# Kernel tuning notes

Hardware: AMD Instinct MI355X
Metric: run time of the kernel (lower is better)

Reference implementation:

```python
import jax, jax.numpy as jnp
import numpy as np

N = 20000      # nodes
E = 640000     # edges
HID = 128      # hidden_dim
HEADS = 8
HD = HID // HEADS  # head_dim = 16


def setup_inputs() -> dict:
    key = jax.random.key(0)
    ks = jax.random.split(key, 32)
    s = 1.0 / np.sqrt(HID)
    d = {}
    d["h"] = jax.random.normal(ks[0], (N, HID), jnp.float32)
    d["x"] = jax.random.normal(ks[1], (N, 3), jnp.float32)
    d["src"] = jax.random.randint(ks[2], (E,), 0, N)
    d["dst"] = jax.random.randint(ks[3], (E,), 0, N)
    d["distances"] = jax.random.uniform(ks[4], (E,), jnp.float32)
    d["bpp_edge_bias"] = jax.random.uniform(ks[5], (E,), jnp.float32)
    d["msa_edge_bias"] = jax.random.uniform(ks[6], (E,), jnp.float32)
    d["chem_edge_bias"] = jax.random.uniform(ks[7], (E,), jnp.float32)
    d["relative_offset"] = jax.random.normal(ks[8], (E,), jnp.float32)
    d["chain_break_mask"] = jax.random.uniform(ks[9], (E,), jnp.float32)
    # attention projections (nn.Linear(hidden, hidden): y = x @ W + b)
    for i, nm in enumerate(["Wq", "Wk", "Wv", "Wo"]):
        d[nm] = jax.random.normal(ks[10 + i], (HID, HID), jnp.float32) * s
    for nm in ["bq", "bk", "bv", "bo"]:
        d[nm] = jnp.zeros((HID,), jnp.float32)
    # six Linear(1, heads) edge-bias heads -> weight vector [HEADS] + bias [HEADS]
    for i, nm in enumerate(["dist", "bpp", "msa", "chem", "rel", "chain"]):
        d["w_" + nm] = jax.random.normal(ks[14 + i], (HEADS,), jnp.float32) * 0.1
        d["b_" + nm] = jnp.zeros((HEADS,), jnp.float32)
    # coord_gate: Linear(HID,HID) -> SiLU -> Linear(HID,1) -> Tanh
    d["Wg1"] = jax.random.normal(ks[20], (HID, HID), jnp.float32) * s
    d["bg1"] = jnp.zeros((HID,), jnp.float32)
    d["wg2"] = jax.random.normal(ks[21], (HID, 1), jnp.float32) * s
    d["bg2"] = jnp.zeros((1,), jnp.float32)
    return d


def _edge_bias(feat, w, b):
    # Linear(1, heads) applied to per-edge scalar: [E] -> [E, HEADS]
    return feat[:, None] * w[None, :] + b[None, :]


def reference(h, x, src, dst, distances, bpp_edge_bias, msa_edge_bias,
              chem_edge_bias, relative_offset, chain_break_mask,
              Wq, bq, Wk, bk, Wv, bv, Wo, bo,
              w_dist, b_dist, w_bpp, b_bpp, w_msa, b_msa,
              w_chem, b_chem, w_rel, b_rel, w_chain, b_chain,
              Wg1, bg1, wg2, bg2):
    n = h.shape[0]
    q = (h @ Wq + bq).reshape(n, HEADS, HD)
    k = (h @ Wk + bk).reshape(n, HEADS, HD)
    v = (h @ Wv + bv).reshape(n, HEADS, HD)
    q_src = q[src]   # [E, H, D]
    k_dst = k[dst]
    v_dst = v[dst]
    logits = jnp.einsum('ehd,ehd->eh', q_src, k_dst) / np.sqrt(float(HD))
    logits = (logits
              - _edge_bias(distances * distances, w_dist, b_dist)
              + _edge_bias(bpp_edge_bias, w_bpp, b_bpp)
              + _edge_bias(msa_edge_bias, w_msa, b_msa)
              + _edge_bias(chem_edge_bias, w_chem, b_chem)
              + _edge_bias(relative_offset, w_rel, b_rel)
              + _edge_bias(chain_break_mask, w_chain, b_chain))
    # segment softmax over edges grouped by src node, per head
    m = jax.ops.segment_max(logits, src, num_segments=n)        # [N, H]
    ex = jnp.exp(logits - m[src])                               # [E, H]
    denom = jax.ops.segment_sum(ex, src, num_segments=n)        # [N, H]
    weights = ex / jnp.maximum(denom[src], 1e-9)                # [E, H]
    # weighted scatter-aggregate of values to src nodes
    h_update = jax.ops.segment_sum(v_dst * weights[:, :, None], src,
                                   num_segments=n).reshape(n, HID)
    h_out = h + h_update @ Wo + bo
    # coordinate update
    weights_mean = weights.mean(axis=1)                         # [E]
    disp = jax.ops.segment_sum((x[dst] - x[src]) * weights_mean[:, None],
                               src, num_segments=n)             # [N, 3]
    gate = jnp.tanh(jax.nn.silu(h_out @ Wg1 + bg1) @ wg2 + bg2)  # [N, 1]
    x_out = x + gate * disp
    return h_out, x_out
```

## Files before the change

### kernel.cpp

```cpp
#include <hip/hip_runtime.h>
#include <hip/hip_bf16.h>
#include <hip/hip_fp16.h>

#define N_NODES 20000
#define N_EDGES 640000
#define HID 128
#define HEADS 8
#define HD 16
#define NB_SCAN ((N_NODES + 255) / 256)
#define CH 192
#define QKV_BLOCKS 625
#define PREP_BLOCKS 2
#define NREP 32
#define HIST_OFF (PREP_BLOCKS + QKV_BLOCKS)
#define HIST_BLOCKS 128

typedef __attribute__((ext_vector_type(8))) short bf16x8;
typedef __attribute__((ext_vector_type(4))) float f32x4;
typedef __attribute__((ext_vector_type(2))) float f32x2;
typedef _Float16 half2_t __attribute__((ext_vector_type(2)));

#if __has_builtin(__builtin_amdgcn_cvt_pk_f32_fp8) && __has_builtin(__builtin_amdgcn_cvt_pk_fp8_f32)
#define FP8_FAST 1
#else
#define FP8_FAST 0
#include <hip/hip_fp8.h>
#endif

__device__ __forceinline__ float bflo(unsigned u) {
    union { unsigned i; float f; } x; x.i = u << 16; return x.f;
}
__device__ __forceinline__ float bfhi(unsigned u) {
    union { unsigned i; float f; } x; x.i = u & 0xffff0000u; return x.f;
}
__device__ __forceinline__ float bfu(ushort u) {
    union { unsigned i; float f; } x; x.i = ((unsigned)u) << 16; return x.f;
}
__device__ __forceinline__ ushort f2bu(float f) {
    __hip_bfloat16 b = __float2bfloat16(f);
    union { __hip_bfloat16 b; ushort u; } c; c.b = b; return c.u;
}
__device__ __forceinline__ ushort f2hu(float f) {
    __half hh = __float2half(f);
    union { __half h; ushort u; } c; c.h = hh; return c.u;
}
__device__ __forceinline__ float fdot2h(unsigned a, unsigned b, float c) {
    union { unsigned u; half2_t h; } A, B;
    A.u = a; B.u = b;
#if __has_builtin(__builtin_amdgcn_fdot2)
    return __builtin_amdgcn_fdot2(A.h, B.h, c, false);
#else
    return c + (float)A.h[0] * (float)B.h[0] + (float)A.h[1] * (float)B.h[1];
#endif
}
__device__ __forceinline__ unsigned fp8x4_enc(float a, float b, float c, float d) {
#if FP8_FAST
    unsigned w = (unsigned)__builtin_amdgcn_cvt_pk_fp8_f32(a, b, 0, false);
    w = (unsigned)__builtin_amdgcn_cvt_pk_fp8_f32(c, d, (int)w, true);
    return w;
#else
    __hip_fp8_e4m3 e0(a), e1(b), e2(c), e3(d);
    return (unsigned)e0.__x | ((unsigned)e1.__x << 8) |
           ((unsigned)e2.__x << 16) | ((unsigned)e3.__x << 24);
#endif
}
__device__ __forceinline__ void fp8x4_dec(unsigned p, float* o) {
#if FP8_FAST
    f32x2 lo = __builtin_amdgcn_cvt_pk_f32_fp8((int)p, false);
    f32x2 hi = __builtin_amdgcn_cvt_pk_f32_fp8((int)p, true);
    o[0] = lo[0]; o[1] = lo[1]; o[2] = hi[0]; o[3] = hi[1];
#else
#pragma unroll
    for (int i = 0; i < 4; ++i) {
        unsigned char b = (p >> (8 * i)) & 0xff;
        __hip_fp8_e4m3 e; e.__x = b;
        o[i] = (float)e;
    }
#endif
}

__global__ __launch_bounds__(256) void front_kernel(
        const float* __restrict__ h,
        const float* __restrict__ bq, const float* __restrict__ bk,
        const float* __restrict__ bv,
        ushort* __restrict__ qb, ushort* __restrict__ kb,
        unsigned char* __restrict__ vb8,
        const int* __restrict__ src,
        int* __restrict__ cnt, int* __restrict__ rank,
        const float* __restrict__ Wq, const float* __restrict__ Wk,
        const float* __restrict__ Wv, const float* __restrict__ Wo,
        const float* __restrict__ Wg1, ushort* __restrict__ Wt) {
    __shared__ __align__(16) ushort hs[32 * 136];
    __shared__ __align__(16) ushort ws[128 * 136];
    const int t = threadIdx.x;
    if (blockIdx.x < PREP_BLOCKS) {
        const float* W = (blockIdx.x == 0) ? Wo : Wg1;
        ushort* out = Wt + (size_t)(3 + blockIdx.x) * 16384;
        for (int i = t; i < 16384; i += 256) {
            int k = i >> 7, n = i & 127;
            out[n * 128 + k] = f2bu(W[i]);
        }
    } else if (blockIdx.x < HIST_OFF) {
        const int row0 = (blockIdx.x - PREP_BLOCKS) * 32;
        for (int i = t; i < 4096; i += 256)
            hs[(i >> 7) * 136 + (i & 127)] = f2bu(h[(size_t)row0 * 128 + i]);
        __syncthreads();
        const int w = t >> 6, lane = t & 63;
        const int rt = w >> 1, half = w & 1;
        const int lrow = lane & 15, lkb = (lane >> 4) * 8;
        bf16x8 a[4];
#pragma unroll
        for (int ks = 0; ks < 4; ++ks)
            a[ks] = *reinterpret_cast<const bf16x8*>(&hs[(rt * 16 + lrow) * 136 + ks * 32 + lkb]);
        __syncthreads();
        const int rloc0 = rt * 16 + (lane >> 4) * 4;
#define STAGE_W(WSRC) \
        for (int idx = t; idx < 8192; idx += 256) { \
            const int c = idx & 127, kp = idx >> 7; \
            const float w0 = WSRC[(2 * kp) * 128 + c]; \
            const float w1 = WSRC[(2 * kp + 1) * 128 + c]; \
            *reinterpret_cast<unsigned*>(&ws[c * 136 + 2 * kp]) = \
                (unsigned)f2bu(w0) | ((unsigned)f2bu(w1) << 16); \
        } \
        __syncthreads();
#define MFMA_COL(col, acc) \
        { \
            _Pragma("unroll") \
            for (int ks = 0; ks < 4; ++ks) { \
                bf16x8 b = *reinterpret_cast<const bf16x8*>( \
                    &ws[(col) * 136 + ks * 32 + lkb]); \
                acc = __builtin_amdgcn_mfma_f32_16x16x32_bf16(a[ks], b, acc, 0, 0, 0); \
            } \
        }
#define DO_MAT_F16(WSRC, BIAS, OUT) \
        { \
        STAGE_W(WSRC) \
        for (int ctp = 0; ctp < 4; ++ctp) { \
            const int col = (ctp * 2 + half) * 16 + lrow; \
            f32x4 acc = {0.f, 0.f, 0.f, 0.f}; \
            MFMA_COL(col, acc) \
            const float bias = BIAS[col]; \
            _Pragma("unroll") \
            for (int r = 0; r < 4; ++r) \
                hs[(rloc0 + r) * 128 + col] = f2hu(acc[r] + bias); \
        } \
        __syncthreads(); \
        { \
            uint4* outp = reinterpret_cast<uint4*>(OUT + (size_t)row0 * 128); \
            const uint4* inp = reinterpret_cast<const uint4*>(hs); \
            outp[t] = inp[t]; \
            outp[t + 256] = inp[t + 256]; \
        } \
        __syncthreads(); \
        }
        DO_MAT_F16(Wq, bq, qb)
        DO_MAT_F16(Wk, bk, kb)
        {
        STAGE_W(Wv)
        unsigned char* hsb = reinterpret_cast<unsigned char*>(hs);
        for (int ctp = 0; ctp < 4; ++ctp) {
            const int col = (ctp * 2 + half) * 16 + lrow;
            f32x4 acc = {0.f, 0.f, 0.f, 0.f};
            MFMA_COL(col, acc)
            const float bias = bv[col];
            const unsigned wpk = fp8x4_enc(acc[0] + bias, acc[1] + bias,
                                           acc[2] + bias, acc[3] + bias);
#pragma unroll
            for (int r = 0; r < 4; ++r)
                hsb[(rloc0 + r) * 128 + col] = (unsigned char)((wpk >> (8 * r)) & 0xff);
        }
        __syncthreads();
        {
            uint4* outp = reinterpret_cast<uint4*>(vb8 + (size_t)row0 * 128);
            const uint4* inp = reinterpret_cast<const uint4*>(hs);
            outp[t] = inp[t];
        }
        }
#undef DO_MAT_F16
#undef MFMA_COL
#undef STAGE_W
    } else {
        const int b = blockIdx.x - HIST_OFF;
        for (int e = b * 256 + t; e < N_EDGES; e += HIST_BLOCKS * 256) {
            const int rep = (e >> 8) & (NREP - 1);
            rank[e] = atomicAdd(&cnt[rep * N_NODES + src[e]], 1);
        }
    }
}

__global__ __launch_bounds__(256) void scan1_kernel(const int* __restrict__ cnt,
        int* __restrict__ repOff, int* __restrict__ startp,
        int* __restrict__ blockSums, int* __restrict__ ticket, int n) {
    __shared__ int sd[256];
    __shared__ int lastFlag;
    const int tid = threadIdx.x;
    const int i = blockIdx.x * 256 + tid;
    int running = 0;
    if (i < n) {
#pragma unroll
        for (int r = 0; r < NREP; ++r) {
            int v = cnt[r * N_NODES + i];
            repOff[r * N_NODES + i] = running;
            running += v;
        }
    }
    sd[tid] = running;
    __syncthreads();
#pragma unroll
    for (int off = 1; off < 256; off <<= 1) {
        int tv = (tid >= off) ? sd[tid - off] : 0;
        __syncthreads();
        sd[tid] += tv;
        __syncthreads();
    }
    if (i < n) startp[i] = sd[tid] - running;
    if (tid == 255) {
        atomicExch(&blockSums[blockIdx.x], sd[255]);
        __threadfence();
        lastFlag = (atomicAdd(ticket, 1) == NB_SCAN - 1);
    }
    __syncthreads();
    if (lastFlag) {
        int v = (tid < NB_SCAN) ? atomicAdd(&blockSums[tid], 0) : 0;
        sd[tid] = v;
        __syncthreads();
#pragma unroll
        for (int off = 1; off < 256; off <<= 1) {
            int tv = (tid >= off) ? sd[tid - off] : 0;
            __syncthreads();
            sd[tid] += tv;
            __syncthreads();
        }
        if (tid < NB_SCAN) blockSums[tid] = sd[tid] - v;
        if (tid == 255) blockSums[NB_SCAN] = sd[255];
    }
}

__global__ __launch_bounds__(256) void scatter_kernel(
        const int* __restrict__ src, const int* __restrict__ dst,
        const float* __restrict__ dist, const float* __restrict__ bpp,
        const float* __restrict__ msa, const float* __restrict__ chem,
        const float* __restrict__ rel, const float* __restrict__ chain,
        const float* __restrict__ w_dist, const float* __restrict__ b_dist,
        const float* __restrict__ w_bpp, const float* __restrict__ b_bpp,
        const float* __restrict__ w_msa, const float* __restrict__ b_msa,
        const float* __restrict__ w_chem, const float* __restrict__ b_chem,
        const float* __restrict__ w_rel, const float* __restrict__ b_rel,
        const float* __restrict__ w_chain, const float* __restrict__ b_chain,
        const int* __restrict__ startp, const int* __restrict__ blockSums,
        const int* __restrict__ repOff, const int* __restrict__ rank,
        const float* __restrict__ x,
        uint4* __restrict__ bias16, uint2* __restrict__ meta) {
    const int b = blockIdx.x;
    const int e = b * 256 + threadIdx.x;
    const int s = src[e];
    const int rep = b & (NREP - 1);
    const int pos = startp[s] + blockSums[s >> 8] + repOff[rep * N_NODES + s] + rank[e];
    const int dn = dst[e];
    const float d2 = dist[e] * dist[e];
    const float f_bpp = bpp[e], f_msa = msa[e], f_chem = chem[e];
    const float f_rel = rel[e], f_chain = chain[e];
    ushort o16[8];
#pragma unroll
    for (int hq = 0; hq < 8; ++hq) {
        float bb = -(d2 * w_dist[hq] + b_dist[hq])
                + (f_bpp * w_bpp[hq] + b_bpp[hq])
                + (f_msa * w_msa[hq] + b_msa[hq])
                + (f_chem * w_chem[hq] + b_chem[hq])
                + (f_rel * w_rel[hq] + b_rel[hq])
                + (f_chain * w_chain[hq] + b_chain[hq]);
        o16[hq] = f2bu(bb);
    }
    uint4 b4;
    b4.x = (unsigned)o16[0] | ((unsigned)o16[1] << 16);
    b4.y = (unsigned)o16[2] | ((unsigned)o16[3] << 16);
    b4.z = (unsigned)o16[4] | ((unsigned)o16[5] << 16);
    b4.w = (unsigned)o16[6] | ((unsigned)o16[7] << 16);
    const float* xp = &x[(size_t)dn * 3];
    uint2 mt;
    mt.x = (unsigned)f2bu(xp[0]) | ((unsigned)f2bu(xp[1]) << 16);
    mt.y = (unsigned)f2bu(xp[2]) | ((unsigned)dn << 16);
    bias16[pos] = b4;
    meta[pos]   = mt;
}

__global__ __launch_bounds__(256) void node_kernel(const ushort* __restrict__ qb,
        const ushort* __restrict__ kb, const unsigned char* __restrict__ vb8,
        const uint4* __restrict__ bias16, const uint2* __restrict__ meta,
        const float* __restrict__ x,
        const int* __restrict__ startp, const int* __restrict__ blockSums,
        ushort* __restrict__ hub, float* __restrict__ disp) {
    __shared__ __align__(16) unsigned qLdsU[4 * 64];
    __shared__ float xsLds[12];
    __shared__ int   sLds[5];
    __shared__ ushort dnLds[CH];
    __shared__ float xLds[CH * 3];
    __shared__ ushort pbLds[CH * 8];
    __shared__ float redN[4][32][9];

    const int t = threadIdx.x;
    const int n0 = blockIdx.x * 4;
    const ushort* biasU = reinterpret_cast<const ushort*>(bias16);

    if (t < 64) {
        const uint4 qv = reinterpret_cast<const uint4*>(qb + (size_t)n0 * 128)[t];
        *reinterpret_cast<uint4*>(&qLdsU[t * 4]) = qv;
    }
    if (t < 12) xsLds[t] = x[(size_t)n0 * 3 + t];
    if (t < 5) {
        int idx = n0 + t;
        sLds[t] = (idx < N_NODES) ? (startp[idx] + blockSums[idx >> 8]) : N_EDGES;
    }
    __syncthreads();

    const int S0 = sLds[0], S4 = sLds[4];
    const int s1r = sLds[1], s2r = sLds[2], s3r = sLds[3];

    const int eg = t >> 5;
    const int dq = t & 31;
    const int hh = dq >> 2;
    const int jj = dq & 3;
    const int j3 = (jj < 3) ? jj : 0;

    float acc0[4] = {0,0,0,0}, acc1[4] = {0,0,0,0};
    float acc2[4] = {0,0,0,0}, acc3[4] = {0,0,0,0};
    float den0 = 0, den1 = 0, den2 = 0, den3 = 0;
    float adx0 = 0, adx1 = 0, adx2 = 0, adx3 = 0;

    for (int base = S0; base < S4; base += CH) {
        const int en = min(CH, S4 - base);
        __syncthreads();
        if (t < en) {
            const uint2 mt = meta[base + t];
            dnLds[t] = (ushort)(mt.y >> 16);
            xLds[t * 3 + 0] = bfu((ushort)(mt.x & 0xffff));
            xLds[t * 3 + 1] = bfu((ushort)(mt.x >> 16));
            xLds[t * 3 + 2] = bfu((ushort)(mt.y & 0xffff));
        }
        __syncthreads();
        const int np = en * 8;
#define PA_BODY(P) { \
            const int e = (P) >> 3, ha = (P) & 7; \
            const int ge = base + e; \
            const int m = (ge >= s1r) + (ge >= s2r) + (ge >= s3r); \
            const ushort* krow = kb + (size_t)dnLds[e] * 128 + ha * 16; \
            const uint4 ka = *reinterpret_cast<const uint4*>(krow); \
            const uint4 kb4 = *reinterpret_cast<const uint4*>(krow + 8); \
            const float bias = bfu(biasU[(size_t)base * 8 + (P)]); \
            const unsigned* qrowU = &qLdsU[m * 64 + ha * 8]; \
            const uint4 qa = *reinterpret_cast<const uint4*>(qrowU); \
            const uint4 qb4 = *reinterpret_cast<const uint4*>(qrowU + 4); \
            float s0 = 0.f, s1 = 0.f, s2 = 0.f, s3 = 0.f; \
            s0 = fdot2h(ka.x, qa.x, s0);   s1 = fdot2h(ka.y, qa.y, s1); \
            s2 = fdot2h(ka.z, qa.z, s2);   s3 = fdot2h(ka.w, qa.w, s3); \
            s0 = fdot2h(kb4.x, qb4.x, s0); s1 = fdot2h(kb4.y, qb4.y, s1); \
            s2 = fdot2h(kb4.z, qb4.z, s2); s3 = fdot2h(kb4.w, qb4.w, s3); \
            pbLds[P] = f2bu(__expf(fmaf((s0 + s1) + (s2 + s3), 0.25f, bias))); \
        }
        {
            int p = t;
            for (; p + 256 < np; p += 512) { PA_BODY(p) PA_BODY(p + 256) }
            if (p < np) PA_BODY(p)
        }
#undef PA_BODY
        __syncthreads();
#define PC_BODY(E, ACC, DEN, ADX, XSV) { \
            const float pe = bfu(pbLds[(E) * 8 + hh]); \
            const unsigned vp = *reinterpret_cast<const unsigned*>( \
                vb8 + (size_t)dnLds[E] * 128 + dq * 4); \
            float vd[4]; \
            fp8x4_dec(vp, vd); \
            ACC[0] = fmaf(pe, vd[0], ACC[0]); \
            ACC[1] = fmaf(pe, vd[1], ACC[1]); \
            ACC[2] = fmaf(pe, vd[2], ACC[2]); \
            ACC[3] = fmaf(pe, vd[3], ACC[3]); \
            DEN += pe; \
            ADX = fmaf(pe, xLds[(E) * 3 + j3] - XSV, ADX); \
        }
#define NODE_C(M, ACC, DEN, ADX) { \
            const int lo = max(sLds[M] - base, 0); \
            const int hi = min(sLds[M + 1] - base, en); \
            const float xsv = xsLds[M * 3 + j3]; \
            int e = lo + eg; \
            for (; e + 8 < hi; e += 16) { \
                PC_BODY(e, ACC, DEN, ADX, xsv) \
                PC_BODY(e + 8, ACC, DEN, ADX, xsv) \
            } \
            if (e < hi) PC_BODY(e, ACC, DEN, ADX, xsv) \
        }
        NODE_C(0, acc0, den0, adx0)
        NODE_C(1, acc1, den1, adx1)
        NODE_C(2, acc2, den2, adx2)
        NODE_C(3, acc3, den3, adx3)
#undef NODE_C
#undef PC_BODY
    }

    const int wv = t >> 6, lane = t & 63;
#define RED_M(M, ACC, DEN, ADX) { \
        float r0 = ACC[0], r1 = ACC[1], r2 = ACC[2], r3 = ACC[3]; \
        float rd = DEN, rx = (jj < 3) ? ADX : 0.f; \
        r0 += __shfl_xor(r0, 32); r1 += __shfl_xor(r1, 32); \
        r2 += __shfl_xor(r2, 32); r3 += __shfl_xor(r3, 32); \
        rd += __shfl_xor(rd, 32); rx += __shfl_xor(rx, 32); \
        if (lane < 32) { \
            redN[wv][lane][0] = r0; redN[wv][lane][1] = r1; \
            redN[wv][lane][2] = r2; redN[wv][lane][3] = r3; \
            redN[wv][lane][4] = rd; redN[wv][lane][5] = rx; \
        } \
        __syncthreads(); \
        if (t < 128) { \
            const int dqr = t >> 2, vi = t & 3; \
            float s = redN[0][dqr][vi] + redN[1][dqr][vi] \
                    + redN[2][dqr][vi] + redN[3][dqr][vi]; \
            float d = redN[0][dqr][4] + redN[1][dqr][4] \
                    + redN[2][dqr][4] + redN[3][dqr][4]; \
            hub[(size_t)(n0 + M) * 128 + t] = f2bu(s / fmaxf(d, 1e-9f)); \
        } \
        if (t < 32) { \
            float v = redN[0][t][5] + redN[1][t][5] + redN[2][t][5] + redN[3][t][5]; \
            float d = redN[0][t][4] + redN[1][t][4] + redN[2][t][4] + redN[3][t][4]; \
            float s = v / fmaxf(d, 1e-9f); \
            s += __shfl_xor(s, 4); s += __shfl_xor(s, 8); s += __shfl_xor(s, 16); \
            if (t < 3) disp[(size_t)(n0 + M) * 3 + t] = s * 0.125f; \
        } \
        __syncthreads(); }
    RED_M(0, acc0, den0, adx0)
    RED_M(1, acc1, den1, adx1)
    RED_M(2, acc2, den2, adx2)
    RED_M(3, acc3, den3, adx3)
#undef RED_M
}

__global__ __launch_bounds__(256) void out_kernel(const float* __restrict__ h,
        const float* __restrict__ x, const ushort* __restrict__ hub,
        const ushort* __restrict__ Wt,
        const float* __restrict__ bo, const float* __restrict__ bg1,
        const float* __restrict__ wg2, const float* __restrict__ bg2,
        const float* __restrict__ disp,
        float* __restrict__ hout, float* __restrict__ xout) {
    __shared__ __align__(16) ushort hus[32 * 136];
    __shared__ __align__(16) float hof[32 * 132];
    __shared__ float g1s[32 * 132];
    const int t = threadIdx.x;
    const int row0 = blockIdx.x * 32;
    for (int i8 = t; i8 < 512; i8 += 256) {
        const int row = i8 >> 4, c8 = (i8 & 15) * 8;
        *reinterpret_cast<uint4*>(&hus[row * 136 + c8]) =
            reinterpret_cast<const uint4*>(hub + (size_t)row0 * 128)[i8];
    }
    for (int i4 = t; i4 < 1024; i4 += 256) {
        const int row = i4 >> 5, c4 = (i4 & 31) * 4;
        *reinterpret_cast<float4*>(&hof[row * 132 + c4]) =
            reinterpret_cast<const float4*>(h + (size_t)row0 * 128)[i4];
    }
    __syncthreads();
    const int w = t >> 6, lane = t & 63;
    const int rt = w >> 1, half = w & 1;
    const int lrow = lane & 15, lkb = (lane >> 4) * 8;
    const int rloc = rt * 16 + (lane >> 4) * 4;
    bf16x8 a[4];
#pragma unroll
    for (int ks = 0; ks < 4; ++ks)
        a[ks] = *reinterpret_cast<const bf16x8*>(&hus[(rt * 16 + lrow) * 136 + ks * 32 + lkb]);
    for (int ctp = 0; ctp < 4; ++ctp) {
        const int col = (ctp * 2 + half) * 16 + lrow;
        f32x4 acc = {0.f, 0.f, 0.f, 0.f};
#pragma unroll
        for (int ks = 0; ks < 4; ++ks) {
            bf16x8 b = *reinterpret_cast<const bf16x8*>(&Wt[3 * 16384 + col * 128 + ks * 32 + lkb]);
            acc = __builtin_amdgcn_mfma_f32_16x16x32_bf16(a[ks], b, acc, 0, 0, 0);
        }
        const float bias = bo[col];
#pragma unroll
        for (int r = 0; r < 4; ++r)
            hof[(rloc + r) * 132 + col] += acc[r] + bias;
    }
    __syncthreads();
    for (int i4 = t; i4 < 1024; i4 += 256) {
        const int row = i4 >> 5, c4 = (i4 & 31) * 4;
        *reinterpret_cast<float4*>(hout + (size_t)(row0 + row) * 128 + c4) =
            *reinterpret_cast<const float4*>(&hof[row * 132 + c4]);
    }
    bf16x8 a2[4];
#pragma unroll
    for (int ks = 0; ks < 4; ++ks) {
        const float* fp = &hof[(rt * 16 + lrow) * 132 + ks * 32 + lkb];
        const float4 f0 = *reinterpret_cast<const float4*>(fp);
        const float4 f1 = *reinterpret_cast<const float4*>(fp + 4);
        bf16x8 v;
        v[0] = (short)f2bu(f0.x); v[1] = (short)f2bu(f0.y);
        v[2] = (short)f2bu(f0.z); v[3] = (short)f2bu(f0.w);
        v[4] = (short)f2bu(f1.x); v[5] = (short)f2bu(f1.y);
        v[6] = (short)f2bu(f1.z); v[7] = (short)f2bu(f1.w);
        a2[ks] = v;
    }
    for (int ctp = 0; ctp < 4; ++ctp) {
        const int col = (ctp * 2 + half) * 16 + lrow;
        f32x4 acc = {0.f, 0.f, 0.f, 0.f};
#pragma unroll
        for (int ks = 0; ks < 4; ++ks) {
            bf16x8 b = *reinterpret_cast<const bf16x8*>(&Wt[4 * 16384 + col * 128 + ks * 32 + lkb]);
            acc = __builtin_amdgcn_mfma_f32_16x16x32_bf16(a2[ks], b, acc, 0, 0, 0);
        }
        const float bias = bg1[col];
#pragma unroll
        for (int r = 0; r < 4; ++r) {
            float av = acc[r] + bias;
            g1s[(rloc + r) * 132 + col] = av / (1.f + __expf(-av));
        }
    }
    __syncthreads();
    {
        const int r = t >> 3, j = t & 7;
        float partial = 0.f;
        for (int cc = j; cc < 128; cc += 8) partial += g1s[r * 132 + cc] * wg2[cc];
        partial += __shfl_xor(partial, 1);
        partial += __shfl_xor(partial, 2);
        partial += __shfl_xor(partial, 4);
        const float gate = tanhf(partial + bg2[0]);
        if (j < 3) {
            const int row = row0 + r;
            xout[(size_t)row * 3 + j] = x[(size_t)row * 3 + j] + gate * disp[(size_t)row * 3 + j];
        }
    }
}


extern "C" void kernel_launch(void* const* d_in, const int* in_sizes, int n_in,
                              void* d_out, int out_size, void* d_ws, size_t ws_size,
                              hipStream_t stream) {
    const float* h     = (const float*)d_in[0];
    const float* x     = (const float*)d_in[1];
    const int*   src   = (const int*)d_in[2];
    const int*   dst   = (const int*)d_in[3];
    const float* dist  = (const float*)d_in[4];
    const float* bpp   = (const float*)d_in[5];
    const float* msa   = (const float*)d_in[6];
    const float* chem  = (const float*)d_in[7];
    const float* rel   = (const float*)d_in[8];
    const float* chain = (const float*)d_in[9];
    const float* Wq = (const float*)d_in[10];
    const float* Wk = (const float*)d_in[11];
    const float* Wv = (const float*)d_in[12];
    const float* Wo = (const float*)d_in[13];
    const float* bq = (const float*)d_in[14];
    const float* bk = (const float*)d_in[15];
    const float* bv = (const float*)d_in[16];
    const float* bo = (const float*)d_in[17];
    const float* w_dist = (const float*)d_in[18];  const float* b_dist = (const float*)d_in[19];
    const float* w_bpp  = (const float*)d_in[20];  const float* b_bpp  = (const float*)d_in[21];
    const float* w_msa  = (const float*)d_in[22];  const float* b_msa  = (const float*)d_in[23];
    const float* w_chem = (const float*)d_in[24];  const float* b_chem = (const float*)d_in[25];
    const float* w_rel  = (const float*)d_in[26];  const float* b_rel  = (const float*)d_in[27];
    const float* w_chain= (const float*)d_in[28];  const float* b_chain= (const float*)d_in[29];
    const float* Wg1 = (const float*)d_in[30];
    const float* bg1 = (const float*)d_in[31];
    const float* wg2 = (const float*)d_in[32];
    const float* bg2 = (const float*)d_in[33];

    char* wp = (char*)d_ws;
    const size_t NH2 = (size_t)N_NODES * HID * sizeof(ushort);
    ushort* hub   = (ushort*)wp;               wp += NH2;
    ushort* qb    = (ushort*)wp;               wp += NH2;
    ushort* kb    = (ushort*)wp;               wp += NH2;
    unsigned char* vb8 = (unsigned char*)wp;   wp += (size_t)N_NODES * HID;
    uint4*  bias16= (uint4*)wp;                wp += (size_t)N_EDGES * 16;
    uint2*  meta  = (uint2*)wp;                wp += (size_t)N_EDGES * 8;
    float*  disp  = (float*)wp;                wp += (size_t)N_NODES * 3 * sizeof(float);
    int* rank     = (int*)wp;                  wp += (size_t)N_EDGES * sizeof(int);
    int* startp   = (int*)wp;                  wp += (size_t)N_NODES * sizeof(int);
    int* cnt      = (int*)wp;                  wp += (size_t)NREP * N_NODES * sizeof(int);
    int* ticket   = (int*)wp;                  wp += sizeof(int);
    int* repOff   = (int*)wp;                  wp += (size_t)NREP * N_NODES * sizeof(int);
    int* blockSums= (int*)wp;                  wp += (size_t)(NB_SCAN + 1) * sizeof(int);
    ushort* Wt    = (ushort*)wp;               wp += (size_t)5 * 16384 * sizeof(ushort);

    float* hout = (float*)d_out;
    float* xout = hout + (size_t)N_NODES * HID;

    hipMemsetAsync(cnt, 0, ((size_t)NREP * N_NODES + 1) * sizeof(int), stream);
    hipLaunchKernelGGL(front_kernel, dim3(HIST_OFF + HIST_BLOCKS), dim3(256), 0, stream,
                       h, bq, bk, bv, qb, kb, vb8,
                       src, cnt, rank, Wq, Wk, Wv, Wo, Wg1, Wt);
    hipLaunchKernelGGL(scan1_kernel, dim3(NB_SCAN), dim3(256), 0, stream,
                       cnt, repOff, startp, blockSums, ticket, N_NODES);
    hipLaunchKernelGGL(scatter_kernel, dim3(N_EDGES / 256), dim3(256), 0, stream,
                       src, dst, dist, bpp, msa, chem, rel, chain,
                       w_dist, b_dist, w_bpp, b_bpp, w_msa, b_msa,
                       w_chem, b_chem, w_rel, b_rel, w_chain, b_chain,
                       startp, blockSums, repOff, rank, x, bias16, meta);
    hipLaunchKernelGGL(node_kernel, dim3(N_NODES / 4), dim3(256), 0, stream,
                       qb, kb, vb8, bias16, meta, x, startp, blockSums, hub, disp);
    hipLaunchKernelGGL(out_kernel, dim3(N_NODES / 32), dim3(256), 0, stream,
                       h, x, hub, Wt, bo, bg1, wg2, bg2, disp, hout, xout);
}
```

Baseline: 134.6 us.

## Pre-transpose QKV weights to bf16 once and read them from global memory

```diff
diff --git a/kernel.cpp b/kernel.cpp
--- a/kernel.cpp
+++ b/kernel.cpp
@@ -10,9 +10,7 @@
 #define NB_SCAN ((N_NODES + 255) / 256)
 #define CH 192
 #define QKV_BLOCKS 625
-#define PREP_BLOCKS 2
 #define NREP 32
-#define HIST_OFF (PREP_BLOCKS + QKV_BLOCKS)
 #define HIST_BLOCKS 128
 
 typedef __attribute__((ext_vector_type(8))) short bf16x8;
@@ -27,12 +25,6 @@
 #include <hip/hip_fp8.h>
 #endif
 
-__device__ __forceinline__ float bflo(unsigned u) {
-    union { unsigned i; float f; } x; x.i = u << 16; return x.f;
-}
-__device__ __forceinline__ float bfhi(unsigned u) {
-    union { unsigned i; float f; } x; x.i = u & 0xffff0000u; return x.f;
-}
 __device__ __forceinline__ float bfu(ushort u) {
     union { unsigned i; float f; } x; x.i = ((unsigned)u) << 16; return x.f;
 }
@@ -79,31 +71,38 @@
 #endif
 }
 
+__global__ __launch_bounds__(256) void prep_kernel(
+        const float* __restrict__ Wq, const float* __restrict__ Wk,
+        const float* __restrict__ Wv, const float* __restrict__ Wo,
+        const float* __restrict__ Wg1, ushort* __restrict__ Wt) {
+    const float* srcs[5] = {Wq, Wk, Wv, Wo, Wg1};
+    const float* W = srcs[blockIdx.x];
+    ushort* out = Wt + (size_t)blockIdx.x * 16384;
+    for (int i = threadIdx.x; i < 16384; i += 256) {
+        int k = i >> 7, n = i & 127;
+        out[n * 128 + k] = f2bu(W[i]);
+    }
+}
+
 __global__ __launch_bounds__(256) void front_kernel(
-        const float* __restrict__ h,
+        const float* __restrict__ h, const ushort* __restrict__ Wt,
         const float* __restrict__ bq, const float* __restrict__ bk,
         const float* __restrict__ bv,
         ushort* __restrict__ qb, ushort* __restrict__ kb,
         unsigned char* __restrict__ vb8,
         const int* __restrict__ src,
-        int* __restrict__ cnt, int* __restrict__ rank,
-        const float* __restrict__ Wq, const float* __restrict__ Wk,
-        const float* __restrict__ Wv, const float* __restrict__ Wo,
-        const float* __restrict__ Wg1, ushort* __restrict__ Wt) {
+        int* __restrict__ cnt, int* __restrict__ rank) {
     __shared__ __align__(16) ushort hs[32 * 136];
-    __shared__ __align__(16) ushort ws[128 * 136];
     const int t = threadIdx.x;
-    if (blockIdx.x < PREP_BLOCKS) {
-        const float* W = (blockIdx.x == 0) ? Wo : Wg1;
-        ushort* out = Wt + (size_t)(3 + blockIdx.x) * 16384;
-        for (int i = t; i < 16384; i += 256) {
-            int k = i >> 7, n = i & 127;
-            out[n * 128 + k] = f2bu(W[i]);
-        }
-    } else if (blockIdx.x < HIST_OFF) {
-        const int row0 = (blockIdx.x - PREP_BLOCKS) * 32;
-        for (int i = t; i < 4096; i += 256)
-            hs[(i >> 7) * 136 + (i & 127)] = f2bu(h[(size_t)row0 * 128 + i]);
+    if (blockIdx.x < QKV_BLOCKS) {
+        const int row0 = blockIdx.x * 32;
+        for (int i4 = t; i4 < 1024; i4 += 256) {
+            const int row = i4 >> 5, c4 = (i4 & 31) * 4;
+            const float4 hv = reinterpret_cast<const float4*>(h + (size_t)row0 * 128)[i4];
+            ushort* dstp = &hs[row * 136 + c4];
+            dstp[0] = f2bu(hv.x); dstp[1] = f2bu(hv.y);
+            dstp[2] = f2bu(hv.z); dstp[3] = f2bu(hv.w);
+        }
         __syncthreads();
         const int w = t >> 6, lane = t & 63;
         const int rt = w >> 1, half = w & 1;
@@ -114,31 +113,21 @@
             a[ks] = *reinterpret_cast<const bf16x8*>(&hs[(rt * 16 + lrow) * 136 + ks * 32 + lkb]);
         __syncthreads();
         const int rloc0 = rt * 16 + (lane >> 4) * 4;
-#define STAGE_W(WSRC) \
-        for (int idx = t; idx < 8192; idx += 256) { \
-            const int c = idx & 127, kp = idx >> 7; \
-            const float w0 = WSRC[(2 * kp) * 128 + c]; \
-            const float w1 = WSRC[(2 * kp + 1) * 128 + c]; \
-            *reinterpret_cast<unsigned*>(&ws[c * 136 + 2 * kp]) = \
-                (unsigned)f2bu(w0) | ((unsigned)f2bu(w1) << 16); \
-        } \
-        __syncthreads();
-#define MFMA_COL(col, acc) \
+#define MFMA_COL(MI, col, acc) \
         { \
             _Pragma("unroll") \
             for (int ks = 0; ks < 4; ++ks) { \
                 bf16x8 b = *reinterpret_cast<const bf16x8*>( \
-                    &ws[(col) * 136 + ks * 32 + lkb]); \
+                    &Wt[(MI) * 16384 + (col) * 128 + ks * 32 + lkb]); \
                 acc = __builtin_amdgcn_mfma_f32_16x16x32_bf16(a[ks], b, acc, 0, 0, 0); \
             } \
         }
-#define DO_MAT_F16(WSRC, BIAS, OUT) \
+#define DO_MAT_F16(MI, BIAS, OUT) \
         { \
-        STAGE_W(WSRC) \
         for (int ctp = 0; ctp < 4; ++ctp) { \
             const int col = (ctp * 2 + half) * 16 + lrow; \
             f32x4 acc = {0.f, 0.f, 0.f, 0.f}; \
-            MFMA_COL(col, acc) \
+            MFMA_COL(MI, col, acc) \
             const float bias = BIAS[col]; \
             _Pragma("unroll") \
             for (int r = 0; r < 4; ++r) \
@@ -153,15 +142,14 @@
         } \
         __syncthreads(); \
         }
-        DO_MAT_F16(Wq, bq, qb)
-        DO_MAT_F16(Wk, bk, kb)
+        DO_MAT_F16(0, bq, qb)
+        DO_MAT_F16(1, bk, kb)
         {
-        STAGE_W(Wv)
         unsigned char* hsb = reinterpret_cast<unsigned char*>(hs);
         for (int ctp = 0; ctp < 4; ++ctp) {
             const int col = (ctp * 2 + half) * 16 + lrow;
             f32x4 acc = {0.f, 0.f, 0.f, 0.f};
-            MFMA_COL(col, acc)
+            MFMA_COL(2, col, acc)
             const float bias = bv[col];
             const unsigned wpk = fp8x4_enc(acc[0] + bias, acc[1] + bias,
                                            acc[2] + bias, acc[3] + bias);
@@ -178,9 +166,8 @@
         }
 #undef DO_MAT_F16
 #undef MFMA_COL
-#undef STAGE_W
     } else {
-        const int b = blockIdx.x - HIST_OFF;
+        const int b = blockIdx.x - QKV_BLOCKS;
         for (int e = b * 256 + t; e < N_EDGES; e += HIST_BLOCKS * 256) {
             const int rep = (e >> 8) & (NREP - 1);
             rank[e] = atomicAdd(&cnt[rep * N_NODES + src[e]], 1);
@@ -580,9 +567,10 @@
     float* xout = hout + (size_t)N_NODES * HID;
 
     hipMemsetAsync(cnt, 0, ((size_t)NREP * N_NODES + 1) * sizeof(int), stream);
-    hipLaunchKernelGGL(front_kernel, dim3(HIST_OFF + HIST_BLOCKS), dim3(256), 0, stream,
-                       h, bq, bk, bv, qb, kb, vb8,
-                       src, cnt, rank, Wq, Wk, Wv, Wo, Wg1, Wt);
+    hipLaunchKernelGGL(prep_kernel, dim3(5), dim3(256), 0, stream,
+                       Wq, Wk, Wv, Wo, Wg1, Wt);
+    hipLaunchKernelGGL(front_kernel, dim3(QKV_BLOCKS + HIST_BLOCKS), dim3(256), 0, stream,
+                       h, Wt, bq, bk, bv, qb, kb, vb8, src, cnt, rank);
     hipLaunchKernelGGL(scan1_kernel, dim3(NB_SCAN), dim3(256), 0, stream,
                        cnt, repOff, startp, blockSums, ticket, N_NODES);
     hipLaunchKernelGGL(scatter_kernel, dim3(N_EDGES / 256), dim3(256), 0, stream,
```

Result: slower. 159.4 us (+18.5%).
